# Kernel optimization log

Hardware: AMD Instinct MI355X
Metric: run time of the kernel (lower is better)

The kernel has to match this reference:

```python
import jax, jax.numpy as jnp
import numpy as np

B, N, D = 8, 256, 128
LN_EPS = 1e-5


def setup_inputs() -> dict:
    key = jax.random.key(0)
    ks = jax.random.split(key, 12)
    s = 0.02
    return {
        "node_features": jax.random.normal(ks[0], (B, N, D), dtype=jnp.float32),
        "adjacency": jax.random.uniform(ks[1], (B, N, N), dtype=jnp.float32),
        "msg_w1": jax.random.normal(ks[2], (2 * D, D), dtype=jnp.float32) * s,
        "msg_b1": jnp.zeros((D,), jnp.float32),
        "msg_w2": jax.random.normal(ks[3], (D, D), dtype=jnp.float32) * s,
        "msg_b2": jnp.zeros((D,), jnp.float32),
        "upd_w1": jax.random.normal(ks[4], (2 * D, D), dtype=jnp.float32) * s,
        "upd_b1": jnp.zeros((D,), jnp.float32),
        "upd_w2": jax.random.normal(ks[5], (D, D), dtype=jnp.float32) * s,
        "upd_b2": jnp.zeros((D,), jnp.float32),
        "ln_g": jnp.ones((D,), jnp.float32),
        "ln_b": jnp.zeros((D,), jnp.float32),
    }


def reference(node_features, adjacency, msg_w1, msg_b1, msg_w2, msg_b2,
              upd_w1, upd_b1, upd_w2, upd_b2, ln_g, ln_b):
    d = node_features.shape[-1]
    n = node_features.shape[1]
    # Split the concat-then-matmul: cat(x_i, x_j) @ W1 == x_i @ W1[:d] + x_j @ W1[d:]
    hi = node_features @ msg_w1[:d]          # [B,N,D] (receiver i contribution)
    hj = node_features @ msg_w1[d:]          # [B,N,D] (sender j contribution)
    h = jax.nn.relu(hi[:, :, None, :] + hj[:, None, :, :] + msg_b1)  # [B,N,N,D]
    # Edge weights with the i==j pairs excluded (loop skips self-edges)
    a = adjacency * (1.0 - jnp.eye(n, dtype=adjacency.dtype))        # [B,N,N]
    # sum_j (h @ W2 + b2) * a_ij  ==  (sum_j h * a_ij) @ W2 + b2 * sum_j a_ij
    s = jnp.einsum('bijd,bij->bid', h, a)    # [B,N,D]
    agg = s @ msg_w2 + msg_b2 * jnp.sum(a, axis=-1, keepdims=True)   # [B,N,D]
    u = jnp.concatenate([node_features, agg], axis=-1)               # [B,N,2D]
    upd = jax.nn.relu(u @ upd_w1 + upd_b1) @ upd_w2 + upd_b2         # [B,N,D]
    res = node_features + upd
    mu = jnp.mean(res, axis=-1, keepdims=True)
    var = jnp.var(res, axis=-1, keepdims=True)
    return (res - mu) / jnp.sqrt(var + LN_EPS) * ln_g + ln_b
```

## Files before the change

### kernel.cpp

```cpp
#include <hip/hip_runtime.h>

#define BB 8
#define NN 256
#define DD 128
#define LN_EPS 1e-5f

__global__ __launch_bounds__(512, 2) void k_proj(const float* __restrict__ x,
                                                 const float* __restrict__ w1,
                                                 const float* __restrict__ b1,
                                                 float* __restrict__ hi,
                                                 float* __restrict__ hjb) {
    __shared__ float xs[4 * DD];
    __shared__ float part[8192];
    const int bid  = blockIdx.x;
    const int row0 = (bid & 7) * NN + (bid >> 3) * 4;
    const int tid  = threadIdx.x;
    xs[tid] = x[row0 * DD + tid];
    __syncthreads();

    const int dp = tid & 127;
    const int kg = tid >> 7;
    const int kb = kg * 32;

    float aA[4] = {}, aB[4] = {};
    #pragma unroll
    for (int k4 = 0; k4 < 8; ++k4) {
        const int k0 = kb + k4 * 4;
        float wa[4], wb[4];
        #pragma unroll
        for (int q = 0; q < 4; ++q) {
            wa[q] = w1[(k0 + q) * DD + dp];
            wb[q] = w1[(DD + k0 + q) * DD + dp];
        }
        #pragma unroll
        for (int r = 0; r < 4; ++r) {
            const float4 xv = *(const float4*)&xs[r * DD + k0];
            aA[r] = fmaf(xv.x, wa[0], aA[r]);
            aA[r] = fmaf(xv.y, wa[1], aA[r]);
            aA[r] = fmaf(xv.z, wa[2], aA[r]);
            aA[r] = fmaf(xv.w, wa[3], aA[r]);
            aB[r] = fmaf(xv.x, wb[0], aB[r]);
            aB[r] = fmaf(xv.y, wb[1], aB[r]);
            aB[r] = fmaf(xv.z, wb[2], aB[r]);
            aB[r] = fmaf(xv.w, wb[3], aB[r]);
        }
    }
    #pragma unroll
    for (int r = 0; r < 4; ++r) {
        part[kg * 512 + r * DD + dp]        = aA[r];
        part[4096 + kg * 512 + r * DD + dp] = aB[r];
    }
    __syncthreads();
    {
        int r = tid >> 7, d = tid & 127;
        float sa = 0.f, sb = 0.f;
        #pragma unroll
        for (int w = 0; w < 4; ++w) {
            sa += part[w * 512 + r * DD + d];
            sb += part[4096 + w * 512 + r * DD + d];
        }
        hi [(row0 + r) * DD + d] = sa;
        hjb[(row0 + r) * DD + d] = sb + b1[d];
    }
}

__global__ __launch_bounds__(1024, 4) void k_fused(const float* __restrict__ adj,
                                                   const float* __restrict__ x,
                                                   const float* __restrict__ hi,
                                                   const float* __restrict__ hjb,
                                                   const float* __restrict__ w2,
                                                   const float* __restrict__ b2,
                                                   const float* __restrict__ w3,
                                                   const float* __restrict__ b3,
                                                   const float* __restrict__ w4,
                                                   const float* __restrict__ b4,
                                                   const float* __restrict__ g,
                                                   const float* __restrict__ bet,
                                                   float* __restrict__ out) {
    extern __shared__ float smem[];
    float* const hall   = smem;
    float* const partP  = smem;
    float* const partT  = smem;
    float* const a_t    = smem + 32768;
    float* const u1s    = smem + 32768;
    float* const resS   = smem + 33792;
    float* const xs     = smem + 34816;
    float* const ssp    = smem + 35840;
    float* const aggs   = smem + 36864;
    float* const asum_s = smem + 37888;

    const int bid = blockIdx.x;
    const int b   = bid & 7;
    const int i0  = (bid >> 3) * 8;
    const int tid = threadIdx.x;

    {
        const float4* src = (const float4*)(hjb + ((size_t)b * NN) * DD);
        float4* dst = (float4*)hall;
        #pragma unroll
        for (int t = 0; t < 8; ++t) dst[tid + t * 1024] = src[tid + t * 1024];
    }
    #pragma unroll
    for (int t = 0; t < 2; ++t) {
        int idx = tid + t * 1024;
        int il = idx >> 8, j = idx & 255;
        int ig = i0 + il;
        float av = adj[((size_t)b * NN + ig) * NN + j];
        a_t[il * 256 + j] = (j == ig) ? 0.f : av;
    }
    xs[tid] = x[((size_t)b * NN + i0) * DD + tid];
    __syncthreads();

    if (tid < 512) {
        int r = tid >> 6, l = tid & 63;
        float s = a_t[r * 256 + l] + a_t[r * 256 + l + 64]
                + a_t[r * 256 + l + 128] + a_t[r * 256 + l + 192];
        #pragma unroll
        for (int m = 32; m; m >>= 1) s += __shfl_xor(s, m);
        if (l == 0) asum_s[r] = s;
    }

    const int dq  = tid & 31;
    const int row = (tid >> 5) & 7;
    const int jh  = tid >> 8;
    const float4 hi4 = *(const float4*)&hi[((size_t)b * NN + i0 + row) * DD + dq * 4];
    float4 acc = {0.f, 0.f, 0.f, 0.f};
    {
        const int j0 = jh * 64;
        #pragma unroll 8
        for (int jj = 0; jj < 64; ++jj) {
            const int j = j0 + jj;
            const float4 hv = *(const float4*)&hall[j * 128 + dq * 4];
            const float a = a_t[row * 256 + j];
            acc.x = fmaf(fmaxf(hi4.x + hv.x, 0.f), a, acc.x);
            acc.y = fmaf(fmaxf(hi4.y + hv.y, 0.f), a, acc.y);
            acc.z = fmaf(fmaxf(hi4.z + hv.z, 0.f), a, acc.z);
            acc.w = fmaf(fmaxf(hi4.w + hv.w, 0.f), a, acc.w);
        }
    }
    __syncthreads();
    *(float4*)&partP[jh * 1024 + row * 128 + dq * 4] = acc;
    __syncthreads();
    {
        float s = partP[tid] + partP[1024 + tid] + partP[2048 + tid] + partP[3072 + tid];
        ssp[tid] = s;
    }
    __syncthreads();

    const int dp = tid & 127;
    const int kg = tid >> 7;
    const int kb = kg * 16;

    {
        float w0[16];
        #pragma unroll
        for (int k = 0; k < 16; ++k) w0[k] = w2[(kb + k) * DD + dp];
        #pragma unroll
        for (int r = 0; r < 8; ++r) {
            float a0 = 0.f;
            #pragma unroll
            for (int q = 0; q < 4; ++q) {
                const float4 sv = *(const float4*)&ssp[r * 128 + kb + q * 4];
                a0 = fmaf(sv.x, w0[q*4+0], a0);
                a0 = fmaf(sv.y, w0[q*4+1], a0);
                a0 = fmaf(sv.z, w0[q*4+2], a0);
                a0 = fmaf(sv.w, w0[q*4+3], a0);
            }
            partT[kg * 1024 + r * 128 + dp] = a0;
        }
    }
    __syncthreads();
    {
        int r = tid >> 7, d = tid & 127;
        float s = 0.f;
        #pragma unroll
        for (int w = 0; w < 8; ++w) s += partT[w * 1024 + tid];
        aggs[tid] = s + b2[d] * asum_s[r];
    }
    __syncthreads();

    {
        float wa0[16], wb0[16];
        #pragma unroll
        for (int k = 0; k < 16; ++k) {
            wa0[k] = w3[(kb + k) * DD + dp];
            wb0[k] = w3[(DD + kb + k) * DD + dp];
        }
        #pragma unroll
        for (int r = 0; r < 8; ++r) {
            float a0 = 0.f;
            #pragma unroll
            for (int q = 0; q < 4; ++q) {
                const float4 xv = *(const float4*)&xs[r * 128 + kb + q * 4];
                const float4 av = *(const float4*)&aggs[r * 128 + kb + q * 4];
                a0 = fmaf(xv.x, wa0[q*4+0], a0);
                a0 = fmaf(xv.y, wa0[q*4+1], a0);
                a0 = fmaf(xv.z, wa0[q*4+2], a0);
                a0 = fmaf(xv.w, wa0[q*4+3], a0);
                a0 = fmaf(av.x, wb0[q*4+0], a0);
                a0 = fmaf(av.y, wb0[q*4+1], a0);
                a0 = fmaf(av.z, wb0[q*4+2], a0);
                a0 = fmaf(av.w, wb0[q*4+3], a0);
            }
            partT[kg * 1024 + r * 128 + dp] = a0;
        }
    }
    __syncthreads();
    {
        int d = tid & 127;
        float s = 0.f;
        #pragma unroll
        for (int w = 0; w < 8; ++w) s += partT[w * 1024 + tid];
        u1s[tid] = fmaxf(s + b3[d], 0.f);
    }
    __syncthreads();

    {
        float w0[16];
        #pragma unroll
        for (int k = 0; k < 16; ++k) w0[k] = w4[(kb + k) * DD + dp];
        #pragma unroll
        for (int r = 0; r < 8; ++r) {
            float a0 = 0.f;
            #pragma unroll
            for (int q = 0; q < 4; ++q) {
                const float4 uv = *(const float4*)&u1s[r * 128 + kb + q * 4];
                a0 = fmaf(uv.x, w0[q*4+0], a0);
                a0 = fmaf(uv.y, w0[q*4+1], a0);
                a0 = fmaf(uv.z, w0[q*4+2], a0);
                a0 = fmaf(uv.w, w0[q*4+3], a0);
            }
            partT[kg * 1024 + r * 128 + dp] = a0;
        }
    }
    __syncthreads();
    {
        int d = tid & 127;
        float s = xs[tid] + b4[d];
        #pragma unroll
        for (int w = 0; w < 8; ++w) s += partT[w * 1024 + tid];
        resS[tid] = s;
    }
    __syncthreads();

    if (tid < 512) {
        const int r = tid >> 6, l = tid & 63;
        const float2 v = *(const float2*)&resS[r * 128 + l * 2];
        float s1 = v.x + v.y;
        float s2 = v.x * v.x + v.y * v.y;
        #pragma unroll
        for (int m = 32; m; m >>= 1) {
            s1 += __shfl_xor(s1, m);
            s2 += __shfl_xor(s2, m);
        }
        const float mu = s1 * (1.f / DD);
        const float rs = rsqrtf(s2 * (1.f / DD) - mu * mu + LN_EPS);
        const int d = l * 2;
        const float2 gv = *(const float2*)&g[d];
        const float2 bv = *(const float2*)&bet[d];
        float2 o;
        o.x = (v.x - mu) * rs * gv.x + bv.x;
        o.y = (v.y - mu) * rs * gv.y + bv.y;
        *(float2*)&out[((size_t)b * NN + i0 + r) * DD + d] = o;
    }
}

extern "C" void kernel_launch(void* const* d_in, const int* in_sizes, int n_in,
                              void* d_out, int out_size, void* d_ws, size_t ws_size,
                              hipStream_t stream) {
    (void)in_sizes; (void)n_in; (void)out_size; (void)ws_size;
    const float* x      = (const float*)d_in[0];
    const float* adj    = (const float*)d_in[1];
    const float* msg_w1 = (const float*)d_in[2];
    const float* msg_b1 = (const float*)d_in[3];
    const float* msg_w2 = (const float*)d_in[4];
    const float* msg_b2 = (const float*)d_in[5];
    const float* upd_w1 = (const float*)d_in[6];
    const float* upd_b1 = (const float*)d_in[7];
    const float* upd_w2 = (const float*)d_in[8];
    const float* upd_b2 = (const float*)d_in[9];
    const float* ln_g   = (const float*)d_in[10];
    const float* ln_b   = (const float*)d_in[11];
    float* out = (float*)d_out;

    const size_t BND = (size_t)BB * NN * DD;
    float* ws  = (float*)d_ws;
    float* hi  = ws;
    float* hjb = ws + BND;

    const size_t dyn_lds = 37896 * sizeof(float);
    hipFuncSetAttribute((const void*)k_fused,
                        hipFuncAttributeMaxDynamicSharedMemorySize,
                        (int)dyn_lds);

    k_proj<<<dim3(512), dim3(512), 0, stream>>>(x, msg_w1, msg_b1, hi, hjb);
    k_fused<<<dim3(256), dim3(1024), dyn_lds, stream>>>(adj, x, hi, hjb,
                                                        msg_w2, msg_b2,
                                                        upd_w1, upd_b1,
                                                        upd_w2, upd_b2,
                                                        ln_g, ln_b, out);
}
```

Before: 25.17 us.

## Register-block two rows per thread in edge aggregation and fuse adjacency row sums

Each thread in the message-aggregation loop now handles two receiver rows, so every LDS load of an hj vector feeds two rows of FMAs. The thread-to-work map changes from 4 j-slices of 64 to 8 j-slices of 32. The adjacency tile is stored transposed so both rows' weights come from a single float2 read. Row sums of the adjacency are computed during the load with wave shuffles instead of in a separate pass. The cost is more partial sums to reduce (8 slices instead of 4) and higher register pressure.

```diff
diff --git a/kernel.cpp b/kernel.cpp
--- a/kernel.cpp
+++ b/kernel.cpp
@@ -81,18 +81,20 @@
     float* const hall   = smem;
     float* const partP  = smem;
     float* const partT  = smem;
-    float* const a_t    = smem + 32768;
+    float* const a_tt   = smem + 32768;
     float* const u1s    = smem + 32768;
     float* const resS   = smem + 33792;
     float* const xs     = smem + 34816;
     float* const ssp    = smem + 35840;
     float* const aggs   = smem + 36864;
-    float* const asum_s = smem + 37888;
+    float* const asub   = smem + 37888;
+    float* const asum_s = smem + 37920;
 
     const int bid = blockIdx.x;
     const int b   = bid & 7;
     const int i0  = (bid >> 3) * 8;
     const int tid = threadIdx.x;
+    const int lane = tid & 63;
 
     {
         const float4* src = (const float4*)(hjb + ((size_t)b * NN) * DD);
@@ -106,43 +108,54 @@
         int il = idx >> 8, j = idx & 255;
         int ig = i0 + il;
         float av = adj[((size_t)b * NN + ig) * NN + j];
-        a_t[il * 256 + j] = (j == ig) ? 0.f : av;
+        av = (j == ig) ? 0.f : av;
+        a_tt[j * 8 + il] = av;
+        float s = av;
+        #pragma unroll
+        for (int m = 32; m; m >>= 1) s += __shfl_xor(s, m);
+        if (lane == 0) asub[il * 4 + ((idx >> 6) & 3)] = s;
     }
     xs[tid] = x[((size_t)b * NN + i0) * DD + tid];
     __syncthreads();
 
-    if (tid < 512) {
-        int r = tid >> 6, l = tid & 63;
-        float s = a_t[r * 256 + l] + a_t[r * 256 + l + 64]
-                + a_t[r * 256 + l + 128] + a_t[r * 256 + l + 192];
-        #pragma unroll
-        for (int m = 32; m; m >>= 1) s += __shfl_xor(s, m);
-        if (l == 0) asum_s[r] = s;
-    }
-
-    const int dq  = tid & 31;
-    const int row = (tid >> 5) & 7;
-    const int jh  = tid >> 8;
-    const float4 hi4 = *(const float4*)&hi[((size_t)b * NN + i0 + row) * DD + dq * 4];
-    float4 acc = {0.f, 0.f, 0.f, 0.f};
-    {
-        const int j0 = jh * 64;
+    if (tid < 8)
+        asum_s[tid] = asub[tid * 4] + asub[tid * 4 + 1]
+                    + asub[tid * 4 + 2] + asub[tid * 4 + 3];
+
+    const int dq = tid & 31;
+    const int rg = (tid >> 5) & 3;
+    const int js = tid >> 7;
+    const float4 hi0 = *(const float4*)&hi[((size_t)b * NN + i0 + rg * 2) * DD + dq * 4];
+    const float4 hi1 = *(const float4*)&hi[((size_t)b * NN + i0 + rg * 2 + 1) * DD + dq * 4];
+    float4 acc0 = {0.f, 0.f, 0.f, 0.f}, acc1 = {0.f, 0.f, 0.f, 0.f};
+    {
+        const int j0 = js * 32;
         #pragma unroll 8
-        for (int jj = 0; jj < 64; ++jj) {
+        for (int jj = 0; jj < 32; ++jj) {
             const int j = j0 + jj;
             const float4 hv = *(const float4*)&hall[j * 128 + dq * 4];
-            const float a = a_t[row * 256 + j];
-            acc.x = fmaf(fmaxf(hi4.x + hv.x, 0.f), a, acc.x);
-            acc.y = fmaf(fmaxf(hi4.y + hv.y, 0.f), a, acc.y);
-            acc.z = fmaf(fmaxf(hi4.z + hv.z, 0.f), a, acc.z);
-            acc.w = fmaf(fmaxf(hi4.w + hv.w, 0.f), a, acc.w);
-        }
-    }
-    __syncthreads();
-    *(float4*)&partP[jh * 1024 + row * 128 + dq * 4] = acc;
-    __syncthreads();
-    {
-        float s = partP[tid] + partP[1024 + tid] + partP[2048 + tid] + partP[3072 + tid];
+            const float2 a2 = *(const float2*)&a_tt[j * 8 + rg * 2];
+            acc0.x = fmaf(fmaxf(hi0.x + hv.x, 0.f), a2.x, acc0.x);
+            acc0.y = fmaf(fmaxf(hi0.y + hv.y, 0.f), a2.x, acc0.y);
+            acc0.z = fmaf(fmaxf(hi0.z + hv.z, 0.f), a2.x, acc0.z);
+            acc0.w = fmaf(fmaxf(hi0.w + hv.w, 0.f), a2.x, acc0.w);
+            acc1.x = fmaf(fmaxf(hi1.x + hv.x, 0.f), a2.y, acc1.x);
+            acc1.y = fmaf(fmaxf(hi1.y + hv.y, 0.f), a2.y, acc1.y);
+            acc1.z = fmaf(fmaxf(hi1.z + hv.z, 0.f), a2.y, acc1.z);
+            acc1.w = fmaf(fmaxf(hi1.w + hv.w, 0.f), a2.y, acc1.w);
+        }
+    }
+    __syncthreads();
+    {
+        float* pp = partP + js * 1024 + (rg * 2) * 128 + dq * 4;
+        *(float4*)(pp)       = acc0;
+        *(float4*)(pp + 128) = acc1;
+    }
+    __syncthreads();
+    {
+        float s = 0.f;
+        #pragma unroll
+        for (int w = 0; w < 8; ++w) s += partP[w * 1024 + tid];
         ssp[tid] = s;
     }
     __syncthreads();
@@ -288,7 +301,7 @@
     float* hi  = ws;
     float* hjb = ws + BND;
 
-    const size_t dyn_lds = 37896 * sizeof(float);
+    const size_t dyn_lds = 37928 * sizeof(float);
     hipFuncSetAttribute((const void*)k_fused,
                         hipFuncAttributeMaxDynamicSharedMemorySize,
                         (int)dyn_lds);
```

After: 27.05 us. +7.4%, slower.
